# Kernel optimization log

Measured on AMD Instinct MI355X. Metric: run time of the kernel, lower is better.

## Reference

```python
import jax, jax.numpy as jnp
import numpy as np

N_NODES = 50000
N_EDGES = 800000
IN_DIM = 64
HID = 64
NUM_GRAPHS = 512


def _gcn_conv(x, W, b, row, col, norm, n):
    # PyG GCNConv: h = x @ W; out[col] += norm * h[row]; out += b
    h = x @ W  # [N, HID]
    msg = h[row] * norm[:, None]  # [E', HID]
    out = jax.ops.segment_sum(msg, col, num_segments=n)
    return out + b


def setup_inputs() -> dict:
    key = jax.random.key(0)
    ks = jax.random.split(key, 12)
    x = jax.random.normal(ks[0], (N_NODES, IN_DIM), dtype=jnp.float32)
    edge_index = jax.random.randint(ks[1], (2, N_EDGES), 0, N_NODES, dtype=jnp.int64)
    batch = jnp.sort(jax.random.randint(ks[2], (N_NODES,), 0, NUM_GRAPHS, dtype=jnp.int64))
    s = 0.05
    W1 = jax.random.normal(ks[3], (IN_DIM, HID), dtype=jnp.float32) * s
    b1 = jnp.zeros((HID,), dtype=jnp.float32)
    W2 = jax.random.normal(ks[4], (HID, HID), dtype=jnp.float32) * s
    b2 = jnp.zeros((HID,), dtype=jnp.float32)
    W3 = jax.random.normal(ks[5], (HID, HID), dtype=jnp.float32) * s
    b3 = jnp.zeros((HID,), dtype=jnp.float32)
    lin_W = jax.random.normal(ks[6], (HID, 1), dtype=jnp.float32) * s
    lin_b = jnp.zeros((1,), dtype=jnp.float32)
    return {"x": x, "W1": W1, "b1": b1, "W2": W2, "b2": b2, "W3": W3,
            "b3": b3, "lin_W": lin_W, "lin_b": lin_b,
            "edge_index": edge_index, "batch": batch}


def reference(x, W1, b1, W2, b2, W3, b3, lin_W, lin_b, edge_index, batch):
    n = x.shape[0]
    # add self-loops (GCNConv default add_self_loops=True)
    loop = jnp.arange(n, dtype=edge_index.dtype)
    row = jnp.concatenate([edge_index[0], loop])  # source
    col = jnp.concatenate([edge_index[1], loop])  # target (aggregation index)
    # symmetric degree normalization: deg over targets with unit weights
    deg = jax.ops.segment_sum(jnp.ones_like(col, dtype=x.dtype), col, num_segments=n)
    dinv = jnp.where(deg > 0, jax.lax.rsqrt(deg), 0.0)
    norm = dinv[row] * dinv[col]  # [E+N]

    h = jax.nn.relu(_gcn_conv(x, W1, b1, row, col, norm, n))
    h = jax.nn.relu(_gcn_conv(h, W2, b2, row, col, norm, n))
    h = _gcn_conv(h, W3, b3, row, col, norm, n)

    # global_mean_pool over batch ids
    sums = jax.ops.segment_sum(h, batch, num_segments=NUM_GRAPHS)
    cnt = jax.ops.segment_sum(jnp.ones((n,), dtype=h.dtype), batch, num_segments=NUM_GRAPHS)
    pooled = sums / jnp.maximum(cnt, 1.0)[:, None]
    # dropout p=0.5 is identity in eval mode
    return pooled @ lin_W + lin_b  # [NUM_GRAPHS, 1]
```

## Files before the change

### kernel.cpp

```cpp
#include <hip/hip_runtime.h>
#include <hip/hip_fp16.h>

#define NN 50000
#define NE 800000
#define HD 64
#define NG 512
#define NBK 196
#define NBL 196
#define M_CNT (NBK * NBL)
#define NBS 151
#define GEMM_BLOCKS 3125


__global__ __launch_bounds__(256) void bucket_count(const int* __restrict__ col,
                                                    const int* __restrict__ batch,
                                                    int* __restrict__ counts,
                                                    int* __restrict__ beg,
                                                    int* __restrict__ endx,
                                                    float* __restrict__ pooled) {
    __shared__ int hist[256];
    int tid = threadIdx.x, blk = blockIdx.x;
    hist[tid] = 0;
    __syncthreads();
    int base = blk * 4096;
#pragma unroll
    for (int k = 0; k < 16; ++k) {
        int e = base + k * 256 + tid;
        if (e < NE) atomicAdd(&hist[col[e] >> 8], 1);
    }
    int t = blk * 256 + tid;
    if (t < NG * HD) pooled[t] = 0.f;
    if (t < NN) {
        int g = batch[t];
        if (t == 0 || batch[t - 1] != g) beg[g] = t;
        if (t == NN - 1 || batch[t + 1] != g) endx[g] = t + 1;
    }
    __syncthreads();
    if (tid < NBK) counts[tid * NBL + blk] = hist[tid];
}

__global__ __launch_bounds__(256) void block_reduce(const int* __restrict__ src,
                                                    int* __restrict__ bsum) {
    __shared__ int ws[4];
    int tid = threadIdx.x, lane = tid & 63, wid = tid >> 6;
    int i = blockIdx.x * 256 + tid;
    int v = (i < M_CNT) ? src[i] : 0;
#pragma unroll
    for (int off = 32; off > 0; off >>= 1) v += __shfl_down(v, off, 64);
    if (lane == 0) ws[wid] = v;
    __syncthreads();
    if (tid == 0) bsum[blockIdx.x] = ws[0] + ws[1] + ws[2] + ws[3];
}

__global__ __launch_bounds__(64) void scan_bsum(int* __restrict__ bsum) {
    int lane = threadIdx.x;
    int carry = 0;
    for (int base = 0; base < NBS; base += 64) {
        int i = base + lane;
        int v = (i < NBS) ? bsum[i] : 0;
        int inc = v;
#pragma unroll
        for (int off = 1; off < 64; off <<= 1) {
            int t = __shfl_up(inc, off, 64);
            if (lane >= off) inc += t;
        }
        if (i < NBS) bsum[i] = carry + inc - v;
        carry += __shfl(inc, 63, 64);
    }
}

__global__ __launch_bounds__(256) void block_scan(const int* __restrict__ src,
                                                  const int* __restrict__ bsum,
                                                  int* __restrict__ dst) {
    __shared__ int ws[4];
    int tid = threadIdx.x, lane = tid & 63, wid = tid >> 6;
    int i = blockIdx.x * 256 + tid;
    int v = (i < M_CNT) ? src[i] : 0;
    int inc = v;
#pragma unroll
    for (int off = 1; off < 64; off <<= 1) {
        int t = __shfl_up(inc, off, 64);
        if (lane >= off) inc += t;
    }
    if (lane == 63) ws[wid] = inc;
    __syncthreads();
    int woff = 0;
    for (int k = 0; k < wid; ++k) woff += ws[k];
    if (i < M_CNT) dst[i] = bsum[blockIdx.x] + woff + inc - v;
}

__global__ __launch_bounds__(256) void gemm1_scatter(const float* __restrict__ x,
                                                     const float* __restrict__ W1,
                                                     float* __restrict__ h32,
                                                     const int* __restrict__ row,
                                                     const int* __restrict__ col,
                                                     const int* __restrict__ counts_ex,
                                                     unsigned* __restrict__ packed) {
    if (blockIdx.x < GEMM_BLOCKS) {
        __shared__ float Ws[64][64];
        __shared__ float Is[16][64];
        int t = threadIdx.x;
        for (int i = t; i < 64 * 64; i += 256) Ws[i >> 6][i & 63] = W1[i];
        int row0 = blockIdx.x * 16;
        for (int i = t; i < 16 * 64; i += 256)
            Is[i >> 6][i & 63] = x[(row0 + (i >> 6)) * HD + (i & 63)];
        __syncthreads();
        int c = t & 63, r4 = t >> 6;
        float a0 = 0.f, a1 = 0.f, a2 = 0.f, a3 = 0.f;
#pragma unroll
        for (int k = 0; k < 64; ++k) {
            float w = Ws[k][c];
            a0 += Is[r4 + 0][k] * w;
            a1 += Is[r4 + 4][k] * w;
            a2 += Is[r4 + 8][k] * w;
            a3 += Is[r4 + 12][k] * w;
        }
        h32[(row0 + r4 + 0) * HD + c] = a0;
        h32[(row0 + r4 + 4) * HD + c] = a1;
        h32[(row0 + r4 + 8) * HD + c] = a2;
        h32[(row0 + r4 + 12) * HD + c] = a3;
    } else {
        __shared__ int cur[256];
        int tid = threadIdx.x, blk = blockIdx.x - GEMM_BLOCKS;
        cur[tid] = 0;
        __syncthreads();
        int base = blk * 4096;
#pragma unroll
        for (int k = 0; k < 16; ++k) {
            int e = base + k * 256 + tid;
            if (e < NE) {
                int c = col[e], r = row[e];
                int b = c >> 8;
                int lpos = atomicAdd(&cur[b], 1);
                int pos = counts_ex[b * NBL + blk] + lpos;
                packed[pos] = (unsigned)r | ((unsigned)(c & 255) << 16);
            }
        }
    }
}

__global__ __launch_bounds__(256) void csr_build(const unsigned* __restrict__ packed,
                                                 const int* __restrict__ counts_ex,
                                                 int* __restrict__ rowptr,
                                                 float* __restrict__ dinv,
                                                 const float* __restrict__ h32,
                                                 __half* __restrict__ h16,
                                                 int* __restrict__ esrc) {
    __shared__ int hist[256];
    __shared__ int ws[4];
    __shared__ int lrp[256];
    __shared__ float sdinv[256];
    int bkt = blockIdx.x, tid = threadIdx.x;
    int s = counts_ex[bkt * NBL];
    int e = (bkt == NBK - 1) ? NE : counts_ex[(bkt + 1) * NBL];
    hist[tid] = 0;
    __syncthreads();
    for (int j = s + tid; j < e; j += 256)
        atomicAdd(&hist[(packed[j] >> 16) & 255], 1);
    __syncthreads();
    int lane = tid & 63, wid = tid >> 6;
    int v = hist[tid], inc = v;
#pragma unroll
    for (int off = 1; off < 64; off <<= 1) {
        int t = __shfl_up(inc, off, 64);
        if (lane >= off) inc += t;
    }
    if (lane == 63) ws[wid] = inc;
    __syncthreads();
    int woff = 0;
    for (int k = 0; k < wid; ++k) woff += ws[k];
    int excl = s + woff + inc - v;
    int node = bkt * 256 + tid;
    float dv = rsqrtf((float)(v + 1));
    if (node < NN) {
        rowptr[node] = excl;
        dinv[node] = dv;
    }
    if (bkt == 0 && tid == 0) rowptr[NN] = NE;
    lrp[tid] = excl;
    sdinv[tid] = dv;
    hist[tid] = 0;
    __syncthreads();
    {
        int nrows = (bkt == NBK - 1) ? (NN - 195 * 256) : 256;
        const float2* hb32 = (const float2*)(h32 + (size_t)bkt * 256 * HD);
        __half2* hb16 = (__half2*)(h16 + (size_t)bkt * 256 * HD);
        for (int i = tid; i < nrows * 32; i += 256) {
            float d = sdinv[i >> 5];
            float2 f = hb32[i];
            hb16[i] = __floats2half2_rn(d * f.x, d * f.y);
        }
    }
    for (int j = s + tid; j < e; j += 256) {
        unsigned p = packed[j];
        int lc = (p >> 16) & 255;
        int slot = lrp[lc] + atomicAdd(&hist[lc], 1);
        esrc[slot] = (int)(p & 0xFFFF);
    }
}

__global__ __launch_bounds__(256) void gemm64_f16(const __half* __restrict__ in,
                                                  const float* __restrict__ W,
                                                  const float* __restrict__ dinv,
                                                  __half* __restrict__ out) {
    __shared__ float Ws[64][64];
    __shared__ float Is[16][64];
    __shared__ float sdinv[16];
    int t = threadIdx.x;
    for (int i = t; i < 64 * 64; i += 256) Ws[i >> 6][i & 63] = W[i];
    int row0 = blockIdx.x * 16;
    if (t < 16) sdinv[t] = dinv[row0 + t];
    const __half2* in2 = (const __half2*)(in + (size_t)row0 * HD);
    for (int i = t; i < 16 * 32; i += 256) {
        float2 v = __half22float2(in2[i]);
        int r = i >> 5, c2 = (i & 31) * 2;
        Is[r][c2]     = fmaxf(v.x, 0.f);
        Is[r][c2 + 1] = fmaxf(v.y, 0.f);
    }
    __syncthreads();
    int c = t & 63, r4 = t >> 6;
    float a0 = 0.f, a1 = 0.f, a2 = 0.f, a3 = 0.f;
#pragma unroll
    for (int k = 0; k < 64; ++k) {
        float w = Ws[k][c];
        a0 += Is[r4 + 0][k] * w;
        a1 += Is[r4 + 4][k] * w;
        a2 += Is[r4 + 8][k] * w;
        a3 += Is[r4 + 12][k] * w;
    }
    out[(row0 + r4 + 0) * HD + c] = __float2half(a0 * sdinv[r4 + 0]);
    out[(row0 + r4 + 4) * HD + c] = __float2half(a1 * sdinv[r4 + 4]);
    out[(row0 + r4 + 8) * HD + c] = __float2half(a2 * sdinv[r4 + 8]);
    out[(row0 + r4 + 12) * HD + c] = __float2half(a3 * sdinv[r4 + 12]);
}

template <bool POOL>
__global__ __launch_bounds__(256) void gather_mt(const __half* __restrict__ hp,
                                                 const int* __restrict__ rowptr,
                                                 const int* __restrict__ esrc,
                                                 const float* __restrict__ dinv,
                                                 const float* __restrict__ b,
                                                 __half* __restrict__ out16,
                                                 const int* __restrict__ batch,
                                                 float* __restrict__ pooled) {
    int tid = threadIdx.x, lane = tid & 63, wid = tid >> 6;
    int p = lane >> 5, c = lane & 31;
    int node = __builtin_amdgcn_readfirstlane(blockIdx.x * 4 + wid);
    const __half2* hv = (const __half2*)hp;
    int s = rowptr[node], e = rowptr[node + 1];
    float2 acc = {0.f, 0.f};
    int j = s;
    for (; j + 8 <= e; j += 8) {
        int t0 = esrc[j + 0], t1 = esrc[j + 1], t2 = esrc[j + 2], t3 = esrc[j + 3];
        int t4 = esrc[j + 4], t5 = esrc[j + 5], t6 = esrc[j + 6], t7 = esrc[j + 7];
        int a0 = p ? t1 : t0;
        int a1 = p ? t3 : t2;
        int a2 = p ? t5 : t4;
        int a3 = p ? t7 : t6;
        float2 f0 = __half22float2(hv[a0 * 32 + c]);
        float2 f1 = __half22float2(hv[a1 * 32 + c]);
        float2 f2 = __half22float2(hv[a2 * 32 + c]);
        float2 f3 = __half22float2(hv[a3 * 32 + c]);
        acc.x += (f0.x + f1.x) + (f2.x + f3.x);
        acc.y += (f0.y + f1.y) + (f2.y + f3.y);
    }
    if (j < e) {
        int t0 = esrc[j + 0] & 0xFFFF, t1 = esrc[j + 1] & 0xFFFF;
        int t2 = esrc[j + 2] & 0xFFFF, t3 = esrc[j + 3] & 0xFFFF;
        int t4 = esrc[j + 4] & 0xFFFF, t5 = esrc[j + 5] & 0xFFFF;
        int t6 = esrc[j + 6] & 0xFFFF, t7 = esrc[j + 7] & 0xFFFF;
        int i0 = j + p, i1 = j + 2 + p, i2 = j + 4 + p, i3 = j + 6 + p;
        int a0 = p ? t1 : t0;
        int a1 = p ? t3 : t2;
        int a2 = p ? t5 : t4;
        int a3 = p ? t7 : t6;
        a0 = (i0 < e) ? a0 : t0;
        a1 = (i1 < e) ? a1 : t0;
        a2 = (i2 < e) ? a2 : t0;
        a3 = (i3 < e) ? a3 : t0;
        float m0 = (i0 < e) ? 1.f : 0.f;
        float m1 = (i1 < e) ? 1.f : 0.f;
        float m2 = (i2 < e) ? 1.f : 0.f;
        float m3 = (i3 < e) ? 1.f : 0.f;
        float2 f0 = __half22float2(hv[a0 * 32 + c]);
        float2 f1 = __half22float2(hv[a1 * 32 + c]);
        float2 f2 = __half22float2(hv[a2 * 32 + c]);
        float2 f3 = __half22float2(hv[a3 * 32 + c]);
        acc.x += m0 * f0.x + m1 * f1.x + m2 * f2.x + m3 * f3.x;
        acc.y += m0 * f0.y + m1 * f1.y + m2 * f2.y + m3 * f3.y;
    }
    acc.x += __shfl_xor(acc.x, 32, 64);
    acc.y += __shfl_xor(acc.y, 32, 64);
    if (p == 0) {
        float di = dinv[node];
        float2 self = __half22float2(hv[node * 32 + c]);
        float2 bb = ((const float2*)b)[c];
        float vx = di * (acc.x + self.x) + bb.x;
        float vy = di * (acc.y + self.y) + bb.y;
        if (POOL) {
            int g = batch[node];
            atomicAdd(&pooled[g * HD + 2 * c], vx);
            atomicAdd(&pooled[g * HD + 2 * c + 1], vy);
        } else {
            ((__half2*)out16)[node * 32 + c] = __floats2half2_rn(vx, vy);
        }
    }
}

__global__ __launch_bounds__(64) void final_kernel(const float* __restrict__ pooled,
                                                   const int* __restrict__ beg,
                                                   const int* __restrict__ endx,
                                                   const float* __restrict__ lin_W,
                                                   const float* __restrict__ lin_b,
                                                   float* __restrict__ out) {
    int g = blockIdx.x, d = threadIdx.x;
    float cnt = (float)(endx[g] - beg[g]);
    float v = pooled[g * HD + d] / fmaxf(cnt, 1.f) * lin_W[d];
#pragma unroll
    for (int off = 32; off > 0; off >>= 1) v += __shfl_down(v, off, 64);
    if (d == 0) out[g] = v + lin_b[0];
}

extern "C" void kernel_launch(void* const* d_in, const int* in_sizes, int n_in,
                              void* d_out, int out_size, void* d_ws, size_t ws_size,
                              hipStream_t stream) {
    const float* x     = (const float*)d_in[0];
    const float* W1    = (const float*)d_in[1];
    const float* b1    = (const float*)d_in[2];
    const float* W2    = (const float*)d_in[3];
    const float* b2    = (const float*)d_in[4];
    const float* W3    = (const float*)d_in[5];
    const float* b3    = (const float*)d_in[6];
    const float* lin_W = (const float*)d_in[7];
    const float* lin_b = (const float*)d_in[8];
    const int* edge_index = (const int*)d_in[9];
    const int* batch      = (const int*)d_in[10];
    const int* row = edge_index;
    const int* col = edge_index + NE;
    float* out = (float*)d_out;

    float*    h32       = (float*)d_ws;
    __half*   h16       = (__half*)(h32 + (size_t)NN * HD);
    __half*   A16       = h16 + (size_t)NN * HD;
    int*      esrc      = (int*)(A16 + (size_t)NN * HD);
    unsigned* packed    = (unsigned*)(esrc + NE + 64);
    int*      counts    = (int*)(packed + NE);
    int*      counts_ex = counts + M_CNT;
    int*      rowptr    = counts_ex + M_CNT;
    float*    dinv      = (float*)(rowptr + NN + 2);
    int*      bsum      = (int*)(dinv + NN);
    float*    pooled    = (float*)(bsum + 256);
    int*      beg       = (int*)(pooled + NG * HD);
    int*      endx      = beg + NG;

    bucket_count<<<NBL, 256, 0, stream>>>(col, batch, counts, beg, endx, pooled);
    block_reduce<<<NBS, 256, 0, stream>>>(counts, bsum);
    scan_bsum<<<1, 64, 0, stream>>>(bsum);
    block_scan<<<NBS, 256, 0, stream>>>(counts, bsum, counts_ex);
    gemm1_scatter<<<GEMM_BLOCKS + NBL, 256, 0, stream>>>(x, W1, h32, row, col,
                                                         counts_ex, packed);
    csr_build<<<NBK, 256, 0, stream>>>(packed, counts_ex, rowptr, dinv,
                                       h32, h16, esrc);

    const int GB = NN / 4;

    gather_mt<false><<<GB, 256, 0, stream>>>(h16, rowptr, esrc, dinv, b1, A16,
                                             batch, pooled);
    gemm64_f16<<<GEMM_BLOCKS, 256, 0, stream>>>(A16, W2, dinv, h16);
    gather_mt<false><<<GB, 256, 0, stream>>>(h16, rowptr, esrc, dinv, b2, A16,
                                             batch, pooled);
    gemm64_f16<<<GEMM_BLOCKS, 256, 0, stream>>>(A16, W3, dinv, h16);
    gather_mt<true><<<GB, 256, 0, stream>>>(h16, rowptr, esrc, dinv, b3, nullptr,
                                            batch, pooled);

    final_kernel<<<NG, 64, 0, stream>>>(pooled, beg, endx, lin_W, lin_b, out);
}
```

Baseline: 261.7 us.

## Store gathered node features as 8-bit e5m2 bytes to halve gather traffic

Node features that the edge gather reads are now stored as the top byte of their fp16 value (an e5m2-like 8-bit format), rounded, instead of full fp16. The CSR build and the dense layer epilogues write this byte format. The gather kernel is reworked so 16 lanes each read 4 packed bytes per neighbour and 4 neighbours are in flight per group, followed by an extra shuffle reduction stage. This targets the random-access bandwidth of the neighbour aggregation, at the cost of only 2 mantissa bits of precision, which risks exceeding the accuracy tolerance.

```diff
diff --git a/kernel.cpp b/kernel.cpp
--- a/kernel.cpp
+++ b/kernel.cpp
@@ -11,6 +11,18 @@
 #define NBS 151
 #define GEMM_BLOCKS 3125
 
+
+__device__ __forceinline__ unsigned char cv8(float f) {
+    return (unsigned char)((__half_as_ushort(__float2half(f)) + 0x80) >> 8);
+}
+
+__device__ __forceinline__ float4 exp8(unsigned u) {
+    unsigned lo = ((u & 0x00FFu) << 8) | ((u & 0xFF00u) << 16);
+    unsigned hi = ((u & 0xFF0000u) >> 8) | (u & 0xFF000000u);
+    __half2 hlo = *(__half2*)&lo, hhi = *(__half2*)&hi;
+    float2 flo = __half22float2(hlo), fhi = __half22float2(hhi);
+    return make_float4(flo.x, flo.y, fhi.x, fhi.y);
+}
 
 __global__ __launch_bounds__(256) void bucket_count(const int* __restrict__ col,
                                                     const int* __restrict__ batch,
@@ -144,7 +156,7 @@
                                                  int* __restrict__ rowptr,
                                                  float* __restrict__ dinv,
                                                  const float* __restrict__ h32,
-                                                 __half* __restrict__ h16,
+                                                 unsigned char* __restrict__ h8,
                                                  int* __restrict__ esrc) {
     __shared__ int hist[256];
     __shared__ int ws[4];
@@ -183,12 +195,16 @@
     __syncthreads();
     {
         int nrows = (bkt == NBK - 1) ? (NN - 195 * 256) : 256;
-        const float2* hb32 = (const float2*)(h32 + (size_t)bkt * 256 * HD);
-        __half2* hb16 = (__half2*)(h16 + (size_t)bkt * 256 * HD);
-        for (int i = tid; i < nrows * 32; i += 256) {
-            float d = sdinv[i >> 5];
-            float2 f = hb32[i];
-            hb16[i] = __floats2half2_rn(d * f.x, d * f.y);
+        const float4* hb32 = (const float4*)(h32 + (size_t)bkt * 256 * HD);
+        unsigned* hb8 = (unsigned*)(h8 + (size_t)bkt * 256 * HD);
+        for (int i = tid; i < nrows * 16; i += 256) {
+            float d = sdinv[i >> 4];
+            float4 f = hb32[i];
+            unsigned u = (unsigned)cv8(d * f.x) |
+                         ((unsigned)cv8(d * f.y) << 8) |
+                         ((unsigned)cv8(d * f.z) << 16) |
+                         ((unsigned)cv8(d * f.w) << 24);
+            hb8[i] = u;
         }
     }
     for (int j = s + tid; j < e; j += 256) {
@@ -202,7 +218,7 @@
 __global__ __launch_bounds__(256) void gemm64_f16(const __half* __restrict__ in,
                                                   const float* __restrict__ W,
                                                   const float* __restrict__ dinv,
-                                                  __half* __restrict__ out) {
+                                                  unsigned char* __restrict__ out8) {
     __shared__ float Ws[64][64];
     __shared__ float Is[16][64];
     __shared__ float sdinv[16];
@@ -228,14 +244,14 @@
         a2 += Is[r4 + 8][k] * w;
         a3 += Is[r4 + 12][k] * w;
     }
-    out[(row0 + r4 + 0) * HD + c] = __float2half(a0 * sdinv[r4 + 0]);
-    out[(row0 + r4 + 4) * HD + c] = __float2half(a1 * sdinv[r4 + 4]);
-    out[(row0 + r4 + 8) * HD + c] = __float2half(a2 * sdinv[r4 + 8]);
-    out[(row0 + r4 + 12) * HD + c] = __float2half(a3 * sdinv[r4 + 12]);
+    out8[(size_t)(row0 + r4 + 0) * HD + c] = cv8(a0 * sdinv[r4 + 0]);
+    out8[(size_t)(row0 + r4 + 4) * HD + c] = cv8(a1 * sdinv[r4 + 4]);
+    out8[(size_t)(row0 + r4 + 8) * HD + c] = cv8(a2 * sdinv[r4 + 8]);
+    out8[(size_t)(row0 + r4 + 12) * HD + c] = cv8(a3 * sdinv[r4 + 12]);
 }
 
 template <bool POOL>
-__global__ __launch_bounds__(256) void gather_mt(const __half* __restrict__ hp,
+__global__ __launch_bounds__(256) void gather_f8(const unsigned char* __restrict__ h8,
                                                  const int* __restrict__ rowptr,
                                                  const int* __restrict__ esrc,
                                                  const float* __restrict__ dinv,
@@ -244,36 +260,46 @@
                                                  const int* __restrict__ batch,
                                                  float* __restrict__ pooled) {
     int tid = threadIdx.x, lane = tid & 63, wid = tid >> 6;
-    int p = lane >> 5, c = lane & 31;
+    int q = lane >> 4, c4 = lane & 15;
+    bool q0 = (q & 1) != 0, q1 = (q & 2) != 0;
     int node = __builtin_amdgcn_readfirstlane(blockIdx.x * 4 + wid);
-    const __half2* hv = (const __half2*)hp;
+    const unsigned* hw = (const unsigned*)h8;
     int s = rowptr[node], e = rowptr[node + 1];
-    float2 acc = {0.f, 0.f};
+    float4 acc = {0.f, 0.f, 0.f, 0.f};
     int j = s;
-    for (; j + 8 <= e; j += 8) {
-        int t0 = esrc[j + 0], t1 = esrc[j + 1], t2 = esrc[j + 2], t3 = esrc[j + 3];
-        int t4 = esrc[j + 4], t5 = esrc[j + 5], t6 = esrc[j + 6], t7 = esrc[j + 7];
-        int a0 = p ? t1 : t0;
-        int a1 = p ? t3 : t2;
-        int a2 = p ? t5 : t4;
-        int a3 = p ? t7 : t6;
-        float2 f0 = __half22float2(hv[a0 * 32 + c]);
-        float2 f1 = __half22float2(hv[a1 * 32 + c]);
-        float2 f2 = __half22float2(hv[a2 * 32 + c]);
-        float2 f3 = __half22float2(hv[a3 * 32 + c]);
+    for (; j + 16 <= e; j += 16) {
+        int t0 = esrc[j + 0],  t1 = esrc[j + 1],  t2 = esrc[j + 2],  t3 = esrc[j + 3];
+        int t4 = esrc[j + 4],  t5 = esrc[j + 5],  t6 = esrc[j + 6],  t7 = esrc[j + 7];
+        int t8 = esrc[j + 8],  t9 = esrc[j + 9],  ta = esrc[j + 10], tb = esrc[j + 11];
+        int tc = esrc[j + 12], td = esrc[j + 13], te = esrc[j + 14], tf = esrc[j + 15];
+        int a0 = q1 ? (q0 ? t3 : t2) : (q0 ? t1 : t0);
+        int a1 = q1 ? (q0 ? t7 : t6) : (q0 ? t5 : t4);
+        int a2 = q1 ? (q0 ? tb : ta) : (q0 ? t9 : t8);
+        int a3 = q1 ? (q0 ? tf : te) : (q0 ? td : tc);
+        unsigned u0 = hw[a0 * 16 + c4];
+        unsigned u1 = hw[a1 * 16 + c4];
+        unsigned u2 = hw[a2 * 16 + c4];
+        unsigned u3 = hw[a3 * 16 + c4];
+        float4 f0 = exp8(u0), f1 = exp8(u1), f2 = exp8(u2), f3 = exp8(u3);
         acc.x += (f0.x + f1.x) + (f2.x + f3.x);
         acc.y += (f0.y + f1.y) + (f2.y + f3.y);
+        acc.z += (f0.z + f1.z) + (f2.z + f3.z);
+        acc.w += (f0.w + f1.w) + (f2.w + f3.w);
     }
     if (j < e) {
-        int t0 = esrc[j + 0] & 0xFFFF, t1 = esrc[j + 1] & 0xFFFF;
-        int t2 = esrc[j + 2] & 0xFFFF, t3 = esrc[j + 3] & 0xFFFF;
-        int t4 = esrc[j + 4] & 0xFFFF, t5 = esrc[j + 5] & 0xFFFF;
-        int t6 = esrc[j + 6] & 0xFFFF, t7 = esrc[j + 7] & 0xFFFF;
-        int i0 = j + p, i1 = j + 2 + p, i2 = j + 4 + p, i3 = j + 6 + p;
-        int a0 = p ? t1 : t0;
-        int a1 = p ? t3 : t2;
-        int a2 = p ? t5 : t4;
-        int a3 = p ? t7 : t6;
+        int t0 = esrc[j + 0]  & 0xFFFF, t1 = esrc[j + 1]  & 0xFFFF;
+        int t2 = esrc[j + 2]  & 0xFFFF, t3 = esrc[j + 3]  & 0xFFFF;
+        int t4 = esrc[j + 4]  & 0xFFFF, t5 = esrc[j + 5]  & 0xFFFF;
+        int t6 = esrc[j + 6]  & 0xFFFF, t7 = esrc[j + 7]  & 0xFFFF;
+        int t8 = esrc[j + 8]  & 0xFFFF, t9 = esrc[j + 9]  & 0xFFFF;
+        int ta = esrc[j + 10] & 0xFFFF, tb = esrc[j + 11] & 0xFFFF;
+        int tc = esrc[j + 12] & 0xFFFF, td = esrc[j + 13] & 0xFFFF;
+        int te = esrc[j + 14] & 0xFFFF, tf = esrc[j + 15] & 0xFFFF;
+        int a0 = q1 ? (q0 ? t3 : t2) : (q0 ? t1 : t0);
+        int a1 = q1 ? (q0 ? t7 : t6) : (q0 ? t5 : t4);
+        int a2 = q1 ? (q0 ? tb : ta) : (q0 ? t9 : t8);
+        int a3 = q1 ? (q0 ? tf : te) : (q0 ? td : tc);
+        int i0 = j + q, i1 = j + 4 + q, i2 = j + 8 + q, i3 = j + 12 + q;
         a0 = (i0 < e) ? a0 : t0;
         a1 = (i1 < e) ? a1 : t0;
         a2 = (i2 < e) ? a2 : t0;
@@ -282,27 +308,44 @@
         float m1 = (i1 < e) ? 1.f : 0.f;
         float m2 = (i2 < e) ? 1.f : 0.f;
         float m3 = (i3 < e) ? 1.f : 0.f;
-        float2 f0 = __half22float2(hv[a0 * 32 + c]);
-        float2 f1 = __half22float2(hv[a1 * 32 + c]);
-        float2 f2 = __half22float2(hv[a2 * 32 + c]);
-        float2 f3 = __half22float2(hv[a3 * 32 + c]);
+        unsigned u0 = hw[a0 * 16 + c4];
+        unsigned u1 = hw[a1 * 16 + c4];
+        unsigned u2 = hw[a2 * 16 + c4];
+        unsigned u3 = hw[a3 * 16 + c4];
+        float4 f0 = exp8(u0), f1 = exp8(u1), f2 = exp8(u2), f3 = exp8(u3);
         acc.x += m0 * f0.x + m1 * f1.x + m2 * f2.x + m3 * f3.x;
         acc.y += m0 * f0.y + m1 * f1.y + m2 * f2.y + m3 * f3.y;
-    }
+        acc.z += m0 * f0.z + m1 * f1.z + m2 * f2.z + m3 * f3.z;
+        acc.w += m0 * f0.w + m1 * f1.w + m2 * f2.w + m3 * f3.w;
+    }
+    acc.x += __shfl_xor(acc.x, 16, 64);
+    acc.y += __shfl_xor(acc.y, 16, 64);
+    acc.z += __shfl_xor(acc.z, 16, 64);
+    acc.w += __shfl_xor(acc.w, 16, 64);
     acc.x += __shfl_xor(acc.x, 32, 64);
     acc.y += __shfl_xor(acc.y, 32, 64);
-    if (p == 0) {
+    acc.z += __shfl_xor(acc.z, 32, 64);
+    acc.w += __shfl_xor(acc.w, 32, 64);
+    if (q == 0) {
         float di = dinv[node];
-        float2 self = __half22float2(hv[node * 32 + c]);
-        float2 bb = ((const float2*)b)[c];
-        float vx = di * (acc.x + self.x) + bb.x;
-        float vy = di * (acc.y + self.y) + bb.y;
+        float4 self = exp8(hw[node * 16 + c4]);
+        float4 bb = ((const float4*)b)[c4];
+        float v0 = di * (acc.x + self.x) + bb.x;
+        float v1 = di * (acc.y + self.y) + bb.y;
+        float v2 = di * (acc.z + self.z) + bb.z;
+        float v3 = di * (acc.w + self.w) + bb.w;
         if (POOL) {
             int g = batch[node];
-            atomicAdd(&pooled[g * HD + 2 * c], vx);
-            atomicAdd(&pooled[g * HD + 2 * c + 1], vy);
+            float* pg = &pooled[g * HD + 4 * c4];
+            atomicAdd(pg + 0, v0);
+            atomicAdd(pg + 1, v1);
+            atomicAdd(pg + 2, v2);
+            atomicAdd(pg + 3, v3);
         } else {
-            ((__half2*)out16)[node * 32 + c] = __floats2half2_rn(vx, vy);
+            union { struct { __half2 a, b; } h; uint2 u; } cv;
+            cv.h.a = __floats2half2_rn(v0, v1);
+            cv.h.b = __floats2half2_rn(v2, v3);
+            ((uint2*)out16)[(size_t)node * 16 + c4] = cv.u;
         }
     }
 }
@@ -339,19 +382,19 @@
     const int* col = edge_index + NE;
     float* out = (float*)d_out;
 
-    float*    h32       = (float*)d_ws;
-    __half*   h16       = (__half*)(h32 + (size_t)NN * HD);
-    __half*   A16       = h16 + (size_t)NN * HD;
-    int*      esrc      = (int*)(A16 + (size_t)NN * HD);
-    unsigned* packed    = (unsigned*)(esrc + NE + 64);
-    int*      counts    = (int*)(packed + NE);
-    int*      counts_ex = counts + M_CNT;
-    int*      rowptr    = counts_ex + M_CNT;
-    float*    dinv      = (float*)(rowptr + NN + 2);
-    int*      bsum      = (int*)(dinv + NN);
-    float*    pooled    = (float*)(bsum + 256);
-    int*      beg       = (int*)(pooled + NG * HD);
-    int*      endx      = beg + NG;
+    float*         h32       = (float*)d_ws;
+    __half*        A16       = (__half*)(h32 + (size_t)NN * HD);
+    unsigned char* h8        = (unsigned char*)(A16 + (size_t)NN * HD);
+    int*           esrc      = (int*)(h8 + (size_t)NN * HD);
+    unsigned*      packed    = (unsigned*)(esrc + NE + 64);
+    int*           counts    = (int*)(packed + NE);
+    int*           counts_ex = counts + M_CNT;
+    int*           rowptr    = counts_ex + M_CNT;
+    float*         dinv      = (float*)(rowptr + NN + 2);
+    int*           bsum      = (int*)(dinv + NN);
+    float*         pooled    = (float*)(bsum + 256);
+    int*           beg       = (int*)(pooled + NG * HD);
+    int*           endx      = beg + NG;
 
     bucket_count<<<NBL, 256, 0, stream>>>(col, batch, counts, beg, endx, pooled);
     block_reduce<<<NBS, 256, 0, stream>>>(counts, bsum);
@@ -360,17 +403,17 @@
     gemm1_scatter<<<GEMM_BLOCKS + NBL, 256, 0, stream>>>(x, W1, h32, row, col,
                                                          counts_ex, packed);
     csr_build<<<NBK, 256, 0, stream>>>(packed, counts_ex, rowptr, dinv,
-                                       h32, h16, esrc);
+                                       h32, h8, esrc);
 
     const int GB = NN / 4;
 
-    gather_mt<false><<<GB, 256, 0, stream>>>(h16, rowptr, esrc, dinv, b1, A16,
+    gather_f8<false><<<GB, 256, 0, stream>>>(h8, rowptr, esrc, dinv, b1, A16,
                                              batch, pooled);
-    gemm64_f16<<<GEMM_BLOCKS, 256, 0, stream>>>(A16, W2, dinv, h16);
-    gather_mt<false><<<GB, 256, 0, stream>>>(h16, rowptr, esrc, dinv, b2, A16,
+    gemm64_f16<<<GEMM_BLOCKS, 256, 0, stream>>>(A16, W2, dinv, h8);
+    gather_f8<false><<<GB, 256, 0, stream>>>(h8, rowptr, esrc, dinv, b2, A16,
                                              batch, pooled);
-    gemm64_f16<<<GEMM_BLOCKS, 256, 0, stream>>>(A16, W3, dinv, h16);
-    gather_mt<true><<<GB, 256, 0, stream>>>(h16, rowptr, esrc, dinv, b3, nullptr,
+    gemm64_f16<<<GEMM_BLOCKS, 256, 0, stream>>>(A16, W3, dinv, h8);
+    gather_f8<true><<<GB, 256, 0, stream>>>(h8, rowptr, esrc, dinv, b3, nullptr,
                                             batch, pooled);
 
     final_kernel<<<NG, 64, 0, stream>>>(pooled, beg, endx, lin_W, lin_b, out);
```

After: 284.5 us. 8.7% more time.

## Fuse next-layer GEMM into gather epilogue and drop separate GEMM kernels

Applied to the files above, without the earlier changes.

Each gather wavefront now preloads a column of the next layer's weight matrix into registers. After aggregating a node, it applies ReLU into a small shared row buffer and computes the 64-wide matvec, writing the dinv-scaled half-precision features directly. This removes the two gemm64_f16 launches and the intermediate A16 write/read round trip. In exchange, every wavefront reloads the full 64x64 weight matrix from cache, and register pressure rises by 64 floats per lane, which may reduce occupancy for the latency-bound gather.

```diff
diff --git a/kernel.cpp b/kernel.cpp
--- a/kernel.cpp
+++ b/kernel.cpp
@@ -199,54 +199,28 @@
     }
 }
 
-__global__ __launch_bounds__(256) void gemm64_f16(const __half* __restrict__ in,
-                                                  const float* __restrict__ W,
-                                                  const float* __restrict__ dinv,
-                                                  __half* __restrict__ out) {
-    __shared__ float Ws[64][64];
-    __shared__ float Is[16][64];
-    __shared__ float sdinv[16];
-    int t = threadIdx.x;
-    for (int i = t; i < 64 * 64; i += 256) Ws[i >> 6][i & 63] = W[i];
-    int row0 = blockIdx.x * 16;
-    if (t < 16) sdinv[t] = dinv[row0 + t];
-    const __half2* in2 = (const __half2*)(in + (size_t)row0 * HD);
-    for (int i = t; i < 16 * 32; i += 256) {
-        float2 v = __half22float2(in2[i]);
-        int r = i >> 5, c2 = (i & 31) * 2;
-        Is[r][c2]     = fmaxf(v.x, 0.f);
-        Is[r][c2 + 1] = fmaxf(v.y, 0.f);
-    }
-    __syncthreads();
-    int c = t & 63, r4 = t >> 6;
-    float a0 = 0.f, a1 = 0.f, a2 = 0.f, a3 = 0.f;
-#pragma unroll
-    for (int k = 0; k < 64; ++k) {
-        float w = Ws[k][c];
-        a0 += Is[r4 + 0][k] * w;
-        a1 += Is[r4 + 4][k] * w;
-        a2 += Is[r4 + 8][k] * w;
-        a3 += Is[r4 + 12][k] * w;
-    }
-    out[(row0 + r4 + 0) * HD + c] = __float2half(a0 * sdinv[r4 + 0]);
-    out[(row0 + r4 + 4) * HD + c] = __float2half(a1 * sdinv[r4 + 4]);
-    out[(row0 + r4 + 8) * HD + c] = __float2half(a2 * sdinv[r4 + 8]);
-    out[(row0 + r4 + 12) * HD + c] = __float2half(a3 * sdinv[r4 + 12]);
-}
-
 template <bool POOL>
-__global__ __launch_bounds__(256) void gather_mt(const __half* __restrict__ hp,
+__global__ __launch_bounds__(256) void gather_fx(const __half* __restrict__ hp,
                                                  const int* __restrict__ rowptr,
                                                  const int* __restrict__ esrc,
                                                  const float* __restrict__ dinv,
                                                  const float* __restrict__ b,
-                                                 __half* __restrict__ out16,
+                                                 const float* __restrict__ Wnext,
+                                                 __half* __restrict__ hnext,
                                                  const int* __restrict__ batch,
                                                  float* __restrict__ pooled) {
+    __shared__ float rowbuf[4][64];
     int tid = threadIdx.x, lane = tid & 63, wid = tid >> 6;
     int p = lane >> 5, c = lane & 31;
     int node = __builtin_amdgcn_readfirstlane(blockIdx.x * 4 + wid);
     const __half2* hv = (const __half2*)hp;
+
+    float wcol[POOL ? 1 : 64];
+    if (!POOL) {
+#pragma unroll
+        for (int k = 0; k < 64; ++k) wcol[k] = Wnext[k * HD + lane];
+    }
+
     int s = rowptr[node], e = rowptr[node + 1];
     float2 acc = {0.f, 0.f};
     int j = s;
@@ -291,19 +265,34 @@
     }
     acc.x += __shfl_xor(acc.x, 32, 64);
     acc.y += __shfl_xor(acc.y, 32, 64);
-    if (p == 0) {
-        float di = dinv[node];
-        float2 self = __half22float2(hv[node * 32 + c]);
-        float2 bb = ((const float2*)b)[c];
-        float vx = di * (acc.x + self.x) + bb.x;
-        float vy = di * (acc.y + self.y) + bb.y;
-        if (POOL) {
+
+    float di = dinv[node];
+    if (POOL) {
+        if (p == 0) {
+            float2 self = __half22float2(hv[node * 32 + c]);
+            float2 bb = ((const float2*)b)[c];
+            float vx = di * (acc.x + self.x) + bb.x;
+            float vy = di * (acc.y + self.y) + bb.y;
             int g = batch[node];
             atomicAdd(&pooled[g * HD + 2 * c], vx);
             atomicAdd(&pooled[g * HD + 2 * c + 1], vy);
-        } else {
-            ((__half2*)out16)[node * 32 + c] = __floats2half2_rn(vx, vy);
-        }
+        }
+    } else {
+        if (p == 0) {
+            float2 self = __half22float2(hv[node * 32 + c]);
+            float2 bb = ((const float2*)b)[c];
+            rowbuf[wid][2 * c]     = fmaxf(di * (acc.x + self.x) + bb.x, 0.f);
+            rowbuf[wid][2 * c + 1] = fmaxf(di * (acc.y + self.y) + bb.y, 0.f);
+        }
+        float outc = 0.f;
+        const float4* rb4 = (const float4*)&rowbuf[wid][0];
+#pragma unroll
+        for (int jj = 0; jj < 16; ++jj) {
+            float4 r = rb4[jj];
+            outc += r.x * wcol[4 * jj + 0] + r.y * wcol[4 * jj + 1]
+                  + r.z * wcol[4 * jj + 2] + r.w * wcol[4 * jj + 3];
+        }
+        hnext[(size_t)node * HD + lane] = __float2half(di * outc);
     }
 }
 
@@ -340,9 +329,9 @@
     float* out = (float*)d_out;
 
     float*    h32       = (float*)d_ws;
-    __half*   h16       = (__half*)(h32 + (size_t)NN * HD);
-    __half*   A16       = h16 + (size_t)NN * HD;
-    int*      esrc      = (int*)(A16 + (size_t)NN * HD);
+    __half*   h16a      = (__half*)(h32 + (size_t)NN * HD);
+    __half*   h16b      = h16a + (size_t)NN * HD;
+    int*      esrc      = (int*)(h16b + (size_t)NN * HD);
     unsigned* packed    = (unsigned*)(esrc + NE + 64);
     int*      counts    = (int*)(packed + NE);
     int*      counts_ex = counts + M_CNT;
@@ -360,18 +349,16 @@
     gemm1_scatter<<<GEMM_BLOCKS + NBL, 256, 0, stream>>>(x, W1, h32, row, col,
                                                          counts_ex, packed);
     csr_build<<<NBK, 256, 0, stream>>>(packed, counts_ex, rowptr, dinv,
-                                       h32, h16, esrc);
+                                       h32, h16a, esrc);
 
     const int GB = NN / 4;
 
-    gather_mt<false><<<GB, 256, 0, stream>>>(h16, rowptr, esrc, dinv, b1, A16,
-                                             batch, pooled);
-    gemm64_f16<<<GEMM_BLOCKS, 256, 0, stream>>>(A16, W2, dinv, h16);
-    gather_mt<false><<<GB, 256, 0, stream>>>(h16, rowptr, esrc, dinv, b2, A16,
-                                             batch, pooled);
-    gemm64_f16<<<GEMM_BLOCKS, 256, 0, stream>>>(A16, W3, dinv, h16);
-    gather_mt<true><<<GB, 256, 0, stream>>>(h16, rowptr, esrc, dinv, b3, nullptr,
-                                            batch, pooled);
+    gather_fx<false><<<GB, 256, 0, stream>>>(h16a, rowptr, esrc, dinv, b1, W2,
+                                             h16b, batch, pooled);
+    gather_fx<false><<<GB, 256, 0, stream>>>(h16b, rowptr, esrc, dinv, b2, W3,
+                                             h16a, batch, pooled);
+    gather_fx<true><<<GB, 256, 0, stream>>>(h16a, rowptr, esrc, dinv, b3, nullptr,
+                                            nullptr, batch, pooled);
 
     final_kernel<<<NG, 64, 0, stream>>>(pooled, beg, endx, lin_W, lin_b, out);
 }
```

Measured after the change: 260.7 us. No clear change (-0.4%).
